# Performance work log

Hardware: AMD Instinct MI355X
Metric: run time of the kernel (lower is better)

Reference implementation:

```python
import jax, jax.numpy as jnp
import numpy as np

B, T, C, HS = 4, 4096, 1024, 64

def setup_inputs() -> dict:
    key = jax.random.key(0)
    kx, kq, kk, kv = jax.random.split(key, 4)
    x = jax.random.normal(kx, (B, T, C), dtype=jnp.float32)
    s = 1.0 / np.sqrt(C)
    Wq = jax.random.normal(kq, (C, HS), dtype=jnp.float32) * s
    Wk = jax.random.normal(kk, (C, HS), dtype=jnp.float32) * s
    Wv = jax.random.normal(kv, (C, HS), dtype=jnp.float32) * s
    return {"x": x, "Wq": Wq, "Wk": Wk, "Wv": Wv}

def reference(x, Wq, Wk, Wv):
    # q,k,v: [B,T,HS]
    q = jnp.einsum('btc,ch->bth', x, Wq)
    k = jnp.einsum('btc,ch,->bth', x, Wk) if False else jnp.einsum('btc,ch->bth', x, Wk)
    v = jnp.einsum('btc,ch->bth', x, Wv)
    dk = q.shape[-1]
    wei = jnp.einsum('bth,bsh->bts', q, k) * (dk ** -0.5)  # [B,T,T]
    Tq = wei.shape[1]
    causal = jnp.tril(jnp.ones((Tq, Tq), dtype=bool))
    wei = jnp.where(causal, wei, -jnp.inf)
    wei = jax.nn.softmax(wei, axis=-1)
    out = jnp.einsum('bts,bsh->bth', wei, v)  # [B,T,HS]
    return out
```

## Files before the change

### kernel.cpp

```cpp
#include <hip/hip_runtime.h>
#include <stdint.h>

typedef __attribute__((ext_vector_type(8))) short short8v;
typedef __attribute__((ext_vector_type(4))) float float4v;

__device__ __forceinline__ unsigned short f32_to_bf16(float f) {
    union { float f; uint32_t u; } v; v.f = f;
    uint32_t u = v.u;
    u += 0x7FFFu + ((u >> 16) & 1u);
    return (unsigned short)(u >> 16);
}

#define T_LEN 4096
#define C_DIM 1024
#define HSZ 64

__global__ void wt_kernel(const float* __restrict__ Wq, const float* __restrict__ Wk,
                          const float* __restrict__ Wv, unsigned short* __restrict__ Wtp) {
    int idx = blockIdx.x * blockDim.x + threadIdx.x;
    int e    = idx & 7;
    int lane = (idx >> 3) & 63;
    int ks   = (idx >> 9) & 31;
    int ct   = idx >> 14;
    int g = lane >> 4, c = lane & 15;
    int k   = ks * 32 + g * 8 + e;
    int col = (ct & 3) * 16 + c;
    int m   = ct >> 2;
    const float* W = (m == 0) ? Wq : ((m == 1) ? Wk : Wv);
    Wtp[idx] = f32_to_bf16(W[(size_t)k * 64 + col]);
}

#define XCH 264

__global__ __launch_bounds__(512) void qkv_kernel(
    const float* __restrict__ x, const unsigned short* __restrict__ Wtp,
    unsigned short* __restrict__ qo, unsigned short* __restrict__ kp,
    unsigned short* __restrict__ vp)
{
    __shared__ __align__(16) unsigned short xs2[2][32 * XCH];
    __shared__ float part[4][2][3][64][4];

    const int tid = threadIdx.x;
    const int bid = (int)blockIdx.x;
    const int batch = (bid >> 1) & 3;
    const int q0    = bid & 1;
    const int hi    = bid >> 3;
    const int rg    = hi * 2 + q0;
    const int row0  = batch * 4096 + rg * 32;

    const int wave = tid >> 6, lane = tid & 63;
    const int wq = wave & 3, wh = wave >> 2;
    const int g = lane >> 4, c = lane & 15;

    float4 ld[4];
    auto LOADX = [&](int cs) {
        #pragma unroll
        for (int i = 0; i < 4; ++i) {
            int f = i * 512 + tid;
            int row = f >> 6, c4 = f & 63;
            ld[i] = *((const float4*)x + (size_t)(row0 + row) * 256 + cs * 64 + c4);
        }
    };
    auto WRITEX = [&](int buf) {
        #pragma unroll
        for (int i = 0; i < 4; ++i) {
            int f = i * 512 + tid;
            int row = f >> 6, c4 = f & 63;
            union { unsigned short s[4]; uint64_t u; } pk;
            pk.s[0] = f32_to_bf16(ld[i].x); pk.s[1] = f32_to_bf16(ld[i].y);
            pk.s[2] = f32_to_bf16(ld[i].z); pk.s[3] = f32_to_bf16(ld[i].w);
            *(uint64_t*)(&xs2[buf][row * XCH + c4 * 4]) = pk.u;
        }
    };

    LOADX(0);
    WRITEX(0);
    __syncthreads();

    float4v acc[2][3];
    #pragma unroll
    for (int rt = 0; rt < 2; ++rt)
        #pragma unroll
        for (int t = 0; t < 3; ++t) acc[rt][t] = (float4v){0,0,0,0};

    const unsigned short* wp0 = Wtp + (size_t)((wq * 3 + 0) * 32) * 512 + lane * 8;
    const unsigned short* wp1 = Wtp + (size_t)((wq * 3 + 1) * 32) * 512 + lane * 8;
    const unsigned short* wp2 = Wtp + (size_t)((wq * 3 + 2) * 32) * 512 + lane * 8;

    for (int cs = 0; cs < 4; ++cs) {
        if (cs < 3) LOADX(cs + 1);
        const int buf = cs & 1;
        #pragma unroll
        for (int ksi = 0; ksi < 4; ++ksi) {
            const int kc = 2 * ksi + wh;
            const int ks = cs * 8 + kc;
            const int koff = kc * 32 + g * 8;
            short8v a0 = *(const short8v*)(&xs2[buf][(0 * 16 + c) * XCH + koff]);
            short8v a1 = *(const short8v*)(&xs2[buf][(1 * 16 + c) * XCH + koff]);
            short8v b0 = *(const short8v*)(wp0 + (size_t)ks * 512);
            short8v b1 = *(const short8v*)(wp1 + (size_t)ks * 512);
            short8v b2 = *(const short8v*)(wp2 + (size_t)ks * 512);
            acc[0][0] = __builtin_amdgcn_mfma_f32_16x16x32_bf16(a0, b0, acc[0][0], 0, 0, 0);
            acc[0][1] = __builtin_amdgcn_mfma_f32_16x16x32_bf16(a0, b1, acc[0][1], 0, 0, 0);
            acc[0][2] = __builtin_amdgcn_mfma_f32_16x16x32_bf16(a0, b2, acc[0][2], 0, 0, 0);
            acc[1][0] = __builtin_amdgcn_mfma_f32_16x16x32_bf16(a1, b0, acc[1][0], 0, 0, 0);
            acc[1][1] = __builtin_amdgcn_mfma_f32_16x16x32_bf16(a1, b1, acc[1][1], 0, 0, 0);
            acc[1][2] = __builtin_amdgcn_mfma_f32_16x16x32_bf16(a1, b2, acc[1][2], 0, 0, 0);
        }
        if (cs < 3) {
            __syncthreads();
            WRITEX(buf ^ 1);
            __syncthreads();
        }
    }

    __syncthreads();
    if (wh == 1) {
        #pragma unroll
        for (int rt = 0; rt < 2; ++rt)
            #pragma unroll
            for (int t = 0; t < 3; ++t)
                #pragma unroll
                for (int j = 0; j < 4; ++j)
                    part[wq][rt][t][lane][j] = acc[rt][t][j];
    }
    __syncthreads();
    if (wh == 0) {
        #pragma unroll
        for (int rt = 0; rt < 2; ++rt) {
            const int row0t = row0 + rt * 16;
            #pragma unroll
            for (int t = 0; t < 3; ++t) {
                float4v av = acc[rt][t];
                #pragma unroll
                for (int j = 0; j < 4; ++j) av[j] += part[wq][rt][t][lane][j];
                int ct = wq * 3 + t;
                int m = ct >> 2, hcol = (ct & 3) * 16 + c;
                if (m == 2) {
                    const int r0 = row0t + g * 4;
                    const int b  = r0 >> 12;
                    const int s0_ = r0 & 4095;
                    const int t2h = s0_ >> 5;
                    const int gv  = (s0_ >> 3) & 3;
                    const int e0  = s0_ & 7;
                    union { unsigned short s[4]; uint64_t u; } pk;
                    #pragma unroll
                    for (int j = 0; j < 4; ++j) pk.s[j] = f32_to_bf16(av[j]);
                    *(uint64_t*)(vp + (size_t)b * 262144 + t2h * 2048 + (ct & 3) * 512
                                    + (gv * 16 + c) * 8 + e0) = pk.u;
                } else if (m == 1) {
                    const int fbase = ((row0t & 4095) >> 6) * 8 + (((row0t & 4095) >> 4) & 3) * 2 + (hcol >> 5);
                    const int b = row0t >> 12;
                    unsigned short* kb = kp + (size_t)b * 262144 + (size_t)fbase * 512
                                         + (((hcol >> 3) & 3) * 16) * 8 + (hcol & 7);
                    #pragma unroll
                    for (int j = 0; j < 4; ++j)
                        kb[(g * 4 + j) * 8] = f32_to_bf16(av[j]);
                } else {
                    float sc = 0.125f;
                    #pragma unroll
                    for (int j = 0; j < 4; ++j)
                        qo[(size_t)(row0t + g * 4 + j) * 64 + hcol] = f32_to_bf16(av[j] * sc);
                }
            }
        }
    }
}

#define PLD 72

__global__ __launch_bounds__(512) void attn_kernel(
    const unsigned short* __restrict__ qi, const unsigned short* __restrict__ kp,
    const unsigned short* __restrict__ vp, float* __restrict__ out)
{
    __shared__ __align__(16) unsigned short Ps[8][16 * PLD];
    __shared__ float CombO[6][16][64];
    __shared__ float CombM[6][16];
    __shared__ float CombL[6][16];

    const int tid   = threadIdx.x;
    const int wave  = tid >> 6, lane = tid & 63;
    const int qh    = wave & 1, slice = wave >> 1;
    const int g = lane >> 4, c = lane & 15;

    const int bid   = (int)blockIdx.x;
    const int batch = (bid >> 1) & 3;
    const int q0    = bid & 1;
    const int m_    = bid >> 3;
    const int mm    = m_ & 31;
    const int qb = q0 ? ((m_ < 32) ? 2 * mm + 1 : 126 - 2 * mm)
                      : ((m_ < 32) ? 2 * mm     : 127 - 2 * mm);

    const int rbase = qb * 32 + qh * 16;
    const size_t bo  = (size_t)batch * T_LEN * HSZ;
    const size_t bov = (size_t)batch * 262144;

    short8v qf0 = *(const short8v*)(qi + bo + (size_t)(rbase + c) * 64 +  0 + g * 8);
    short8v qf1 = *(const short8v*)(qi + bo + (size_t)(rbase + c) * 64 + 32 + g * 8);

    float4v acc[4];
    #pragma unroll
    for (int i2 = 0; i2 < 4; ++i2) acc[i2] = (float4v){0,0,0,0};
    float mrow = -3e38f;
    float lsum = 0.f;

    const int nt_w = ((rbase + 15) >> 6) + 1;
    unsigned short* Pw = &Ps[wave][0];

    short8v kf[8], kn[8];

    auto TILE = [&](int t, const short8v* kb) {
        const int s0 = t * 64;

        float4v sa[4];
        #pragma unroll
        for (int ct = 0; ct < 4; ++ct) {
            float4v z = {0, 0, 0, 0};
            z = __builtin_amdgcn_mfma_f32_16x16x32_bf16(kb[ct * 2 + 0], qf0, z, 0, 0, 0);
            sa[ct] = __builtin_amdgcn_mfma_f32_16x16x32_bf16(kb[ct * 2 + 1], qf1, z, 0, 0, 0);
        }

        short8v vf0[4];
        #pragma unroll
        for (int dt = 0; dt < 4; ++dt)
            vf0[dt] = *(const short8v*)(vp + bov + (size_t)(t * 8 + dt) * 512 + lane * 8);

        if (s0 + 63 > rbase) {
            #pragma unroll
            for (int ct = 0; ct < 4; ++ct)
                #pragma unroll
                for (int j = 0; j < 4; ++j)
                    if (s0 + ct * 16 + g * 4 + j > rbase + c) sa[ct][j] = -3e38f;
        }

        float mx01 = fmaxf(fmaxf(sa[0][0], sa[0][1]), fmaxf(sa[0][2], sa[0][3]));
        float mx11 = fmaxf(fmaxf(sa[1][0], sa[1][1]), fmaxf(sa[1][2], sa[1][3]));
        float mx21 = fmaxf(fmaxf(sa[2][0], sa[2][1]), fmaxf(sa[2][2], sa[2][3]));
        float mx31 = fmaxf(fmaxf(sa[3][0], sa[3][1]), fmaxf(sa[3][2], sa[3][3]));
        float mx = fmaxf(fmaxf(mx01, mx11), fmaxf(mx21, mx31));
        mx = fmaxf(mx, __shfl_xor(mx, 16, 64));
        mx = fmaxf(mx, __shfl_xor(mx, 32, 64));
        const float nm = fmaxf(mrow, mx);
        const float al = __expf(mrow - nm);
        mrow = nm;
        float ps = 0.f;
        #pragma unroll
        for (int ct = 0; ct < 4; ++ct)
            #pragma unroll
            for (int j = 0; j < 4; ++j) {
                float p = __expf(sa[ct][j] - nm);
                sa[ct][j] = p;
                ps += p;
            }
        lsum = lsum * al + ps;
        #pragma unroll
        for (int dt = 0; dt < 4; ++dt)
            #pragma unroll
            for (int j = 0; j < 4; ++j) acc[dt][j] *= al;

        #pragma unroll
        for (int ct = 0; ct < 4; ++ct) {
            union { unsigned short s[4]; uint64_t u; } pk4;
            #pragma unroll
            for (int j = 0; j < 4; ++j) pk4.s[j] = f32_to_bf16(sa[ct][j]);
            *(uint64_t*)(&Pw[c * PLD + ct * 16 + g * 4]) = pk4.u;
        }

        short8v vf1[4];
        #pragma unroll
        for (int dt = 0; dt < 4; ++dt)
            vf1[dt] = *(const short8v*)(vp + bov + (size_t)(t * 8 + 4 + dt) * 512 + lane * 8);

        short8v pa0 = *(const short8v*)(&Pw[c * PLD +  0 + g * 8]);
        short8v pa1 = *(const short8v*)(&Pw[c * PLD + 32 + g * 8]);

        #pragma unroll
        for (int dt = 0; dt < 4; ++dt)
            acc[dt] = __builtin_amdgcn_mfma_f32_16x16x32_bf16(vf0[dt], pa0, acc[dt], 0, 0, 0);
        #pragma unroll
        for (int dt = 0; dt < 4; ++dt)
            acc[dt] = __builtin_amdgcn_mfma_f32_16x16x32_bf16(vf1[dt], pa1, acc[dt], 0, 0, 0);
    };

    auto LOADK = [&](int t, short8v* kd) {
        #pragma unroll
        for (int f = 0; f < 8; ++f)
            kd[f] = *(const short8v*)(kp + bov + (size_t)(t * 8 + f) * 512 + lane * 8);
    };

    int t = slice;
    if (t < nt_w) {
        LOADK(t, kf);
        while (true) {
            const bool h1 = (t + 4 < nt_w);
            if (h1) LOADK(t + 4, kn);
            TILE(t, kf);
            if (!h1) break;
            t += 4;
            const bool h2 = (t + 4 < nt_w);
            if (h2) LOADK(t + 4, kf);
            TILE(t, kn);
            if (!h2) break;
            t += 4;
        }
    }

    lsum += __shfl_xor(lsum, 16, 64);
    lsum += __shfl_xor(lsum, 32, 64);

    if (slice > 0) {
        const int sidx = (slice - 1) * 2 + qh;
        #pragma unroll
        for (int dt = 0; dt < 4; ++dt)
            #pragma unroll
            for (int j = 0; j < 4; ++j)
                CombO[sidx][c][dt * 16 + g * 4 + j] = acc[dt][j];
        if (g == 0) {
            CombM[sidx][c] = mrow;
            CombL[sidx][c] = lsum;
        }
    }
    __syncthreads();

    if (slice == 0) {
        float M = mrow;
        #pragma unroll
        for (int s = 0; s < 3; ++s) M = fmaxf(M, CombM[s * 2 + qh][c]);
        const float a0 = __expf(mrow - M);
        float as[3];
        float lt = lsum * a0;
        #pragma unroll
        for (int s = 0; s < 3; ++s) {
            as[s] = __expf(CombM[s * 2 + qh][c] - M);
            lt += as[s] * CombL[s * 2 + qh][c];
        }
        const float linv = 1.0f / lt;
        #pragma unroll
        for (int dt = 0; dt < 4; ++dt) {
            float4 o;
            float* op = &o.x;
            #pragma unroll
            for (int j = 0; j < 4; ++j) {
                float v = acc[dt][j] * a0;
                #pragma unroll
                for (int s = 0; s < 3; ++s)
                    v += as[s] * CombO[s * 2 + qh][c][dt * 16 + g * 4 + j];
                op[j] = v * linv;
            }
            *(float4*)(out + bo + (size_t)(rbase + c) * 64 + dt * 16 + g * 4) = o;
        }
    }
}

extern "C" void kernel_launch(void* const* d_in, const int* in_sizes, int n_in,
                              void* d_out, int out_size, void* d_ws, size_t ws_size,
                              hipStream_t stream) {
    const float* x  = (const float*)d_in[0];
    const float* Wq = (const float*)d_in[1];
    const float* Wk = (const float*)d_in[2];
    const float* Wv = (const float*)d_in[3];

    unsigned short* Wt = (unsigned short*)d_ws;
    unsigned short* q  = (unsigned short*)((char*)d_ws + (size_t)3 * 65536 * 2);
    unsigned short* kp = q + (size_t)4 * T_LEN * HSZ;
    unsigned short* vp = kp + (size_t)4 * T_LEN * HSZ;
    float* out = (float*)d_out;

    hipLaunchKernelGGL(wt_kernel,  dim3(768), dim3(256), 0, stream, Wq, Wk, Wv, Wt);
    hipLaunchKernelGGL(qkv_kernel, dim3(512), dim3(512), 0, stream, x, Wt, q, kp, vp);
    hipLaunchKernelGGL(attn_kernel, dim3(512), dim3(512), 0, stream, q, kp, vp, out);
}
```

Before: 52.86 us.

## Process both 16-row query halves per wave, sharing K/V tiles across 8 KV slices

```diff
diff --git a/kernel.cpp b/kernel.cpp
--- a/kernel.cpp
+++ b/kernel.cpp
@@ -9,6 +9,10 @@
     uint32_t u = v.u;
     u += 0x7FFFu + ((u >> 16) & 1u);
     return (unsigned short)(u >> 16);
+}
+__device__ __forceinline__ float bf16_to_f32(unsigned short s) {
+    union { uint32_t u; float f; } v; v.u = ((uint32_t)s) << 16;
+    return v.f;
 }
 
 #define T_LEN 4096
@@ -173,76 +177,59 @@
     const unsigned short* __restrict__ qi, const unsigned short* __restrict__ kp,
     const unsigned short* __restrict__ vp, float* __restrict__ out)
 {
-    __shared__ __align__(16) unsigned short Ps[8][16 * PLD];
-    __shared__ float CombO[6][16][64];
-    __shared__ float CombM[6][16];
-    __shared__ float CombL[6][16];
-
-    const int tid   = threadIdx.x;
-    const int wave  = tid >> 6, lane = tid & 63;
-    const int qh    = wave & 1, slice = wave >> 1;
+    __shared__ __align__(16) unsigned short Ps[8][2][16 * PLD];
+    __shared__ unsigned short CombO[2][7][16][64];
+    __shared__ float CombM[2][7][16];
+    __shared__ float CombL[2][7][16];
+
+    const int tid  = threadIdx.x;
+    const int wave = tid >> 6, lane = tid & 63;
     const int g = lane >> 4, c = lane & 15;
 
     const int bid   = (int)blockIdx.x;
+    const int q0    = bid & 1;
     const int batch = (bid >> 1) & 3;
-    const int q0    = bid & 1;
-    const int m_    = bid >> 3;
-    const int mm    = m_ & 31;
-    const int qb = q0 ? ((m_ < 32) ? 2 * mm + 1 : 126 - 2 * mm)
-                      : ((m_ < 32) ? 2 * mm     : 127 - 2 * mm);
-
-    const int rbase = qb * 32 + qh * 16;
+    const int hi    = bid >> 3;
+    const int qb    = 127 - (2 * hi + q0);
+
+    const int rb0 = qb * 32, rb1 = qb * 32 + 16;
+    const int nt0 = ((rb0 + 15) >> 6) + 1;
+    const int nt1 = ((rb1 + 15) >> 6) + 1;
     const size_t bo  = (size_t)batch * T_LEN * HSZ;
     const size_t bov = (size_t)batch * 262144;
 
-    short8v qf0 = *(const short8v*)(qi + bo + (size_t)(rbase + c) * 64 +  0 + g * 8);
-    short8v qf1 = *(const short8v*)(qi + bo + (size_t)(rbase + c) * 64 + 32 + g * 8);
-
-    float4v acc[4];
+    short8v qf00 = *(const short8v*)(qi + bo + (size_t)(rb0 + c) * 64 +  0 + g * 8);
+    short8v qf01 = *(const short8v*)(qi + bo + (size_t)(rb0 + c) * 64 + 32 + g * 8);
+    short8v qf10 = *(const short8v*)(qi + bo + (size_t)(rb1 + c) * 64 +  0 + g * 8);
+    short8v qf11 = *(const short8v*)(qi + bo + (size_t)(rb1 + c) * 64 + 32 + g * 8);
+
+    float4v acc0[4], acc1[4];
     #pragma unroll
-    for (int i2 = 0; i2 < 4; ++i2) acc[i2] = (float4v){0,0,0,0};
-    float mrow = -3e38f;
-    float lsum = 0.f;
-
-    const int nt_w = ((rbase + 15) >> 6) + 1;
-    unsigned short* Pw = &Ps[wave][0];
+    for (int i = 0; i < 4; ++i) { acc0[i] = (float4v){0,0,0,0}; acc1[i] = (float4v){0,0,0,0}; }
+    float m0 = -3e38f, m1 = -3e38f, l0 = 0.f, l1 = 0.f;
+
+    unsigned short* Pw0 = &Ps[wave][0][0];
+    unsigned short* Pw1 = &Ps[wave][1][0];
 
     short8v kf[8], kn[8];
 
-    auto TILE = [&](int t, const short8v* kb) {
-        const int s0 = t * 64;
-
-        float4v sa[4];
-        #pragma unroll
-        for (int ct = 0; ct < 4; ++ct) {
-            float4v z = {0, 0, 0, 0};
-            z = __builtin_amdgcn_mfma_f32_16x16x32_bf16(kb[ct * 2 + 0], qf0, z, 0, 0, 0);
-            sa[ct] = __builtin_amdgcn_mfma_f32_16x16x32_bf16(kb[ct * 2 + 1], qf1, z, 0, 0, 0);
-        }
-
-        short8v vf0[4];
-        #pragma unroll
-        for (int dt = 0; dt < 4; ++dt)
-            vf0[dt] = *(const short8v*)(vp + bov + (size_t)(t * 8 + dt) * 512 + lane * 8);
-
-        if (s0 + 63 > rbase) {
-            #pragma unroll
-            for (int ct = 0; ct < 4; ++ct)
-                #pragma unroll
-                for (int j = 0; j < 4; ++j)
-                    if (s0 + ct * 16 + g * 4 + j > rbase + c) sa[ct][j] = -3e38f;
-        }
-
-        float mx01 = fmaxf(fmaxf(sa[0][0], sa[0][1]), fmaxf(sa[0][2], sa[0][3]));
-        float mx11 = fmaxf(fmaxf(sa[1][0], sa[1][1]), fmaxf(sa[1][2], sa[1][3]));
-        float mx21 = fmaxf(fmaxf(sa[2][0], sa[2][1]), fmaxf(sa[2][2], sa[2][3]));
-        float mx31 = fmaxf(fmaxf(sa[3][0], sa[3][1]), fmaxf(sa[3][2], sa[3][3]));
-        float mx = fmaxf(fmaxf(mx01, mx11), fmaxf(mx21, mx31));
+    auto LOADK = [&](int t, short8v* kd) {
+        #pragma unroll
+        for (int f = 0; f < 8; ++f)
+            kd[f] = *(const short8v*)(kp + bov + (size_t)(t * 8 + f) * 512 + lane * 8);
+    };
+
+    auto SMAX = [&](float4v* sa, float& mr, float& ls, float4v* ac) {
+        float mxA = fmaxf(fmaxf(sa[0][0], sa[0][1]), fmaxf(sa[0][2], sa[0][3]));
+        float mxB = fmaxf(fmaxf(sa[1][0], sa[1][1]), fmaxf(sa[1][2], sa[1][3]));
+        float mxC = fmaxf(fmaxf(sa[2][0], sa[2][1]), fmaxf(sa[2][2], sa[2][3]));
+        float mxD = fmaxf(fmaxf(sa[3][0], sa[3][1]), fmaxf(sa[3][2], sa[3][3]));
+        float mx = fmaxf(fmaxf(mxA, mxB), fmaxf(mxC, mxD));
         mx = fmaxf(mx, __shfl_xor(mx, 16, 64));
         mx = fmaxf(mx, __shfl_xor(mx, 32, 64));
-        const float nm = fmaxf(mrow, mx);
-        const float al = __expf(mrow - nm);
-        mrow = nm;
+        const float nm = fmaxf(mr, mx);
+        const float al = __expf(mr - nm);
+        mr = nm;
         float ps = 0.f;
         #pragma unroll
         for (int ct = 0; ct < 4; ++ct)
@@ -252,12 +239,14 @@
                 sa[ct][j] = p;
                 ps += p;
             }
-        lsum = lsum * al + ps;
-        #pragma unroll
-        for (int dt = 0; dt < 4; ++dt)
-            #pragma unroll
-            for (int j = 0; j < 4; ++j) acc[dt][j] *= al;
-
+        ls = ls * al + ps;
+        #pragma unroll
+        for (int dt = 0; dt < 4; ++dt)
+            #pragma unroll
+            for (int j = 0; j < 4; ++j) ac[dt][j] *= al;
+    };
+
+    auto PWRITE = [&](unsigned short* Pw, const float4v* sa) {
         #pragma unroll
         for (int ct = 0; ct < 4; ++ct) {
             union { unsigned short s[4]; uint64_t u; } pk4;
@@ -265,74 +254,129 @@
             for (int j = 0; j < 4; ++j) pk4.s[j] = f32_to_bf16(sa[ct][j]);
             *(uint64_t*)(&Pw[c * PLD + ct * 16 + g * 4]) = pk4.u;
         }
+    };
+
+    auto TILE2 = [&](int t, const short8v* kb) {
+        const int s0 = t * 64;
+        const bool h0 = t < nt0;
+
+        float4v sa0[4], sa1[4];
+        if (h0) {
+            #pragma unroll
+            for (int ct = 0; ct < 4; ++ct) {
+                float4v z = {0, 0, 0, 0};
+                z = __builtin_amdgcn_mfma_f32_16x16x32_bf16(kb[ct * 2 + 0], qf00, z, 0, 0, 0);
+                sa0[ct] = __builtin_amdgcn_mfma_f32_16x16x32_bf16(kb[ct * 2 + 1], qf01, z, 0, 0, 0);
+            }
+        }
+        #pragma unroll
+        for (int ct = 0; ct < 4; ++ct) {
+            float4v z = {0, 0, 0, 0};
+            z = __builtin_amdgcn_mfma_f32_16x16x32_bf16(kb[ct * 2 + 0], qf10, z, 0, 0, 0);
+            sa1[ct] = __builtin_amdgcn_mfma_f32_16x16x32_bf16(kb[ct * 2 + 1], qf11, z, 0, 0, 0);
+        }
+
+        short8v vf0[4];
+        #pragma unroll
+        for (int dt = 0; dt < 4; ++dt)
+            vf0[dt] = *(const short8v*)(vp + bov + (size_t)(t * 8 + dt) * 512 + lane * 8);
+
+        if (h0 && s0 + 63 > rb0) {
+            #pragma unroll
+            for (int ct = 0; ct < 4; ++ct)
+                #pragma unroll
+                for (int j = 0; j < 4; ++j)
+                    if (s0 + ct * 16 + g * 4 + j > rb0 + c) sa0[ct][j] = -3e38f;
+        }
+        if (s0 + 63 > rb1) {
+            #pragma unroll
+            for (int ct = 0; ct < 4; ++ct)
+                #pragma unroll
+                for (int j = 0; j < 4; ++j)
+                    if (s0 + ct * 16 + g * 4 + j > rb1 + c) sa1[ct][j] = -3e38f;
+        }
+
+        if (h0) SMAX(sa0, m0, l0, acc0);
+        SMAX(sa1, m1, l1, acc1);
+
+        if (h0) PWRITE(Pw0, sa0);
+        PWRITE(Pw1, sa1);
 
         short8v vf1[4];
         #pragma unroll
         for (int dt = 0; dt < 4; ++dt)
             vf1[dt] = *(const short8v*)(vp + bov + (size_t)(t * 8 + 4 + dt) * 512 + lane * 8);
 
-        short8v pa0 = *(const short8v*)(&Pw[c * PLD +  0 + g * 8]);
-        short8v pa1 = *(const short8v*)(&Pw[c * PLD + 32 + g * 8]);
-
-        #pragma unroll
-        for (int dt = 0; dt < 4; ++dt)
-            acc[dt] = __builtin_amdgcn_mfma_f32_16x16x32_bf16(vf0[dt], pa0, acc[dt], 0, 0, 0);
-        #pragma unroll
-        for (int dt = 0; dt < 4; ++dt)
-            acc[dt] = __builtin_amdgcn_mfma_f32_16x16x32_bf16(vf1[dt], pa1, acc[dt], 0, 0, 0);
-    };
-
-    auto LOADK = [&](int t, short8v* kd) {
-        #pragma unroll
-        for (int f = 0; f < 8; ++f)
-            kd[f] = *(const short8v*)(kp + bov + (size_t)(t * 8 + f) * 512 + lane * 8);
-    };
-
-    int t = slice;
-    if (t < nt_w) {
+        short8v pa10 = *(const short8v*)(&Pw1[c * PLD +  0 + g * 8]);
+        short8v pa11 = *(const short8v*)(&Pw1[c * PLD + 32 + g * 8]);
+        #pragma unroll
+        for (int dt = 0; dt < 4; ++dt)
+            acc1[dt] = __builtin_amdgcn_mfma_f32_16x16x32_bf16(vf0[dt], pa10, acc1[dt], 0, 0, 0);
+        #pragma unroll
+        for (int dt = 0; dt < 4; ++dt)
+            acc1[dt] = __builtin_amdgcn_mfma_f32_16x16x32_bf16(vf1[dt], pa11, acc1[dt], 0, 0, 0);
+
+        if (h0) {
+            short8v pa00 = *(const short8v*)(&Pw0[c * PLD +  0 + g * 8]);
+            short8v pa01 = *(const short8v*)(&Pw0[c * PLD + 32 + g * 8]);
+            #pragma unroll
+            for (int dt = 0; dt < 4; ++dt)
+                acc0[dt] = __builtin_amdgcn_mfma_f32_16x16x32_bf16(vf0[dt], pa00, acc0[dt], 0, 0, 0);
+            #pragma unroll
+            for (int dt = 0; dt < 4; ++dt)
+                acc0[dt] = __builtin_amdgcn_mfma_f32_16x16x32_bf16(vf1[dt], pa01, acc0[dt], 0, 0, 0);
+        }
+    };
+
+    int t = wave;
+    if (t < nt1) {
         LOADK(t, kf);
         while (true) {
-            const bool h1 = (t + 4 < nt_w);
-            if (h1) LOADK(t + 4, kn);
-            TILE(t, kf);
+            const bool h1 = (t + 8 < nt1);
+            if (h1) LOADK(t + 8, kn);
+            TILE2(t, kf);
             if (!h1) break;
-            t += 4;
-            const bool h2 = (t + 4 < nt_w);
-            if (h2) LOADK(t + 4, kf);
-            TILE(t, kn);
+            t += 8;
+            const bool h2 = (t + 8 < nt1);
+            if (h2) LOADK(t + 8, kf);
+            TILE2(t, kn);
             if (!h2) break;
-            t += 4;
-        }
-    }
-
-    lsum += __shfl_xor(lsum, 16, 64);
-    lsum += __shfl_xor(lsum, 32, 64);
-
-    if (slice > 0) {
-        const int sidx = (slice - 1) * 2 + qh;
+            t += 8;
+        }
+    }
+
+    l0 += __shfl_xor(l0, 16, 64); l0 += __shfl_xor(l0, 32, 64);
+    l1 += __shfl_xor(l1, 16, 64); l1 += __shfl_xor(l1, 32, 64);
+
+    if (wave != 0) {
         #pragma unroll
         for (int dt = 0; dt < 4; ++dt)
             #pragma unroll
             for (int j = 0; j < 4; ++j)
-                CombO[sidx][c][dt * 16 + g * 4 + j] = acc[dt][j];
-        if (g == 0) {
-            CombM[sidx][c] = mrow;
-            CombL[sidx][c] = lsum;
-        }
+                CombO[0][wave - 1][c][dt * 16 + g * 4 + j] = f32_to_bf16(acc0[dt][j]);
+        if (g == 0) { CombM[0][wave - 1][c] = m0; CombL[0][wave - 1][c] = l0; }
+    }
+    if (wave != 7) {
+        #pragma unroll
+        for (int dt = 0; dt < 4; ++dt)
+            #pragma unroll
+            for (int j = 0; j < 4; ++j)
+                CombO[1][wave][c][dt * 16 + g * 4 + j] = f32_to_bf16(acc1[dt][j]);
+        if (g == 0) { CombM[1][wave][c] = m1; CombL[1][wave][c] = l1; }
     }
     __syncthreads();
 
-    if (slice == 0) {
-        float M = mrow;
-        #pragma unroll
-        for (int s = 0; s < 3; ++s) M = fmaxf(M, CombM[s * 2 + qh][c]);
-        const float a0 = __expf(mrow - M);
-        float as[3];
-        float lt = lsum * a0;
-        #pragma unroll
-        for (int s = 0; s < 3; ++s) {
-            as[s] = __expf(CombM[s * 2 + qh][c] - M);
-            lt += as[s] * CombL[s * 2 + qh][c];
+    auto FINAL = [&](int h, int rb, const float4v* aw, float mw, float lw) {
+        float M = mw;
+        #pragma unroll
+        for (int s = 0; s < 7; ++s) M = fmaxf(M, CombM[h][s][c]);
+        const float a0 = __expf(mw - M);
+        float as[7];
+        float lt = lw * a0;
+        #pragma unroll
+        for (int s = 0; s < 7; ++s) {
+            as[s] = __expf(CombM[h][s][c] - M);
+            lt += as[s] * CombL[h][s][c];
         }
         const float linv = 1.0f / lt;
         #pragma unroll
@@ -341,15 +385,18 @@
             float* op = &o.x;
             #pragma unroll
             for (int j = 0; j < 4; ++j) {
-                float v = acc[dt][j] * a0;
+                float v = aw[dt][j] * a0;
                 #pragma unroll
-                for (int s = 0; s < 3; ++s)
-                    v += as[s] * CombO[s * 2 + qh][c][dt * 16 + g * 4 + j];
+                for (int s = 0; s < 7; ++s)
+                    v += as[s] * bf16_to_f32(CombO[h][s][c][dt * 16 + g * 4 + j]);
                 op[j] = v * linv;
             }
-            *(float4*)(out + bo + (size_t)(rbase + c) * 64 + dt * 16 + g * 4) = o;
-        }
-    }
+            *(float4*)(out + bo + (size_t)(rb + c) * 64 + dt * 16 + g * 4) = o;
+        }
+    };
+
+    if (wave == 0) FINAL(0, rb0, acc0, m0, l0);
+    if (wave == 7) FINAL(1, rb1, acc1, m1, l1);
 }
 
 extern "C" void kernel_launch(void* const* d_in, const int* in_sizes, int n_in,
```

Measured after the change: 56.32 us. +6.6%, slower.

## Enlarge QKV projection tile to 64 rows and alias partial-sum LDS

Applied to the files above, without the earlier changes.

```diff
diff --git a/kernel.cpp b/kernel.cpp
--- a/kernel.cpp
+++ b/kernel.cpp
@@ -9,6 +9,10 @@
     uint32_t u = v.u;
     u += 0x7FFFu + ((u >> 16) & 1u);
     return (unsigned short)(u >> 16);
+}
+__device__ __forceinline__ float bf16_to_f32(unsigned short s) {
+    union { uint32_t u; float f; } v; v.u = ((uint32_t)s) << 16;
+    return v.f;
 }
 
 #define T_LEN 4096
@@ -30,15 +34,16 @@
     Wtp[idx] = f32_to_bf16(W[(size_t)k * 64 + col]);
 }
 
-#define XCH 264
+#define XCH2 136
 
 __global__ __launch_bounds__(512) void qkv_kernel(
     const float* __restrict__ x, const unsigned short* __restrict__ Wtp,
     unsigned short* __restrict__ qo, unsigned short* __restrict__ kp,
     unsigned short* __restrict__ vp)
 {
-    __shared__ __align__(16) unsigned short xs2[2][32 * XCH];
-    __shared__ float part[4][2][3][64][4];
+    __shared__ __align__(16) char smem[4 * 4 * 3 * 64 * 4 * 4];
+    unsigned short (*xs2)[64 * XCH2] = (unsigned short (*)[64 * XCH2])smem;
+    float* part = (float*)smem;
 
     const int tid = threadIdx.x;
     const int bid = (int)blockIdx.x;
@@ -46,7 +51,7 @@
     const int q0    = bid & 1;
     const int hi    = bid >> 3;
     const int rg    = hi * 2 + q0;
-    const int row0  = batch * 4096 + rg * 32;
+    const int row0  = batch * 4096 + rg * 64;
 
     const int wave = tid >> 6, lane = tid & 63;
     const int wq = wave & 3, wh = wave >> 2;
@@ -57,19 +62,19 @@
         #pragma unroll
         for (int i = 0; i < 4; ++i) {
             int f = i * 512 + tid;
-            int row = f >> 6, c4 = f & 63;
-            ld[i] = *((const float4*)x + (size_t)(row0 + row) * 256 + cs * 64 + c4);
+            int row = f >> 5, c4 = f & 31;
+            ld[i] = *((const float4*)x + (size_t)(row0 + row) * 256 + cs * 32 + c4);
         }
     };
     auto WRITEX = [&](int buf) {
         #pragma unroll
         for (int i = 0; i < 4; ++i) {
             int f = i * 512 + tid;
-            int row = f >> 6, c4 = f & 63;
+            int row = f >> 5, c4 = f & 31;
             union { unsigned short s[4]; uint64_t u; } pk;
             pk.s[0] = f32_to_bf16(ld[i].x); pk.s[1] = f32_to_bf16(ld[i].y);
             pk.s[2] = f32_to_bf16(ld[i].z); pk.s[3] = f32_to_bf16(ld[i].w);
-            *(uint64_t*)(&xs2[buf][row * XCH + c4 * 4]) = pk.u;
+            *(uint64_t*)(&xs2[buf][row * XCH2 + c4 * 4]) = pk.u;
         }
     };
 
@@ -77,9 +82,9 @@
     WRITEX(0);
     __syncthreads();
 
-    float4v acc[2][3];
+    float4v acc[4][3];
     #pragma unroll
-    for (int rt = 0; rt < 2; ++rt)
+    for (int rt = 0; rt < 4; ++rt)
         #pragma unroll
         for (int t = 0; t < 3; ++t) acc[rt][t] = (float4v){0,0,0,0};
 
@@ -87,27 +92,26 @@
     const unsigned short* wp1 = Wtp + (size_t)((wq * 3 + 1) * 32) * 512 + lane * 8;
     const unsigned short* wp2 = Wtp + (size_t)((wq * 3 + 2) * 32) * 512 + lane * 8;
 
-    for (int cs = 0; cs < 4; ++cs) {
-        if (cs < 3) LOADX(cs + 1);
+    for (int cs = 0; cs < 8; ++cs) {
+        if (cs < 7) LOADX(cs + 1);
         const int buf = cs & 1;
         #pragma unroll
-        for (int ksi = 0; ksi < 4; ++ksi) {
+        for (int ksi = 0; ksi < 2; ++ksi) {
             const int kc = 2 * ksi + wh;
-            const int ks = cs * 8 + kc;
+            const int ks = cs * 4 + kc;
             const int koff = kc * 32 + g * 8;
-            short8v a0 = *(const short8v*)(&xs2[buf][(0 * 16 + c) * XCH + koff]);
-            short8v a1 = *(const short8v*)(&xs2[buf][(1 * 16 + c) * XCH + koff]);
             short8v b0 = *(const short8v*)(wp0 + (size_t)ks * 512);
             short8v b1 = *(const short8v*)(wp1 + (size_t)ks * 512);
             short8v b2 = *(const short8v*)(wp2 + (size_t)ks * 512);
-            acc[0][0] = __builtin_amdgcn_mfma_f32_16x16x32_bf16(a0, b0, acc[0][0], 0, 0, 0);
-            acc[0][1] = __builtin_amdgcn_mfma_f32_16x16x32_bf16(a0, b1, acc[0][1], 0, 0, 0);
-            acc[0][2] = __builtin_amdgcn_mfma_f32_16x16x32_bf16(a0, b2, acc[0][2], 0, 0, 0);
-            acc[1][0] = __builtin_amdgcn_mfma_f32_16x16x32_bf16(a1, b0, acc[1][0], 0, 0, 0);
-            acc[1][1] = __builtin_amdgcn_mfma_f32_16x16x32_bf16(a1, b1, acc[1][1], 0, 0, 0);
-            acc[1][2] = __builtin_amdgcn_mfma_f32_16x16x32_bf16(a1, b2, acc[1][2], 0, 0, 0);
-        }
-        if (cs < 3) {
+            #pragma unroll
+            for (int rt = 0; rt < 4; ++rt) {
+                short8v a = *(const short8v*)(&xs2[buf][(rt * 16 + c) * XCH2 + koff]);
+                acc[rt][0] = __builtin_amdgcn_mfma_f32_16x16x32_bf16(a, b0, acc[rt][0], 0, 0, 0);
+                acc[rt][1] = __builtin_amdgcn_mfma_f32_16x16x32_bf16(a, b1, acc[rt][1], 0, 0, 0);
+                acc[rt][2] = __builtin_amdgcn_mfma_f32_16x16x32_bf16(a, b2, acc[rt][2], 0, 0, 0);
+            }
+        }
+        if (cs < 7) {
             __syncthreads();
             WRITEX(buf ^ 1);
             __syncthreads();
@@ -117,23 +121,24 @@
     __syncthreads();
     if (wh == 1) {
         #pragma unroll
-        for (int rt = 0; rt < 2; ++rt)
+        for (int rt = 0; rt < 4; ++rt)
             #pragma unroll
             for (int t = 0; t < 3; ++t)
                 #pragma unroll
                 for (int j = 0; j < 4; ++j)
-                    part[wq][rt][t][lane][j] = acc[rt][t][j];
+                    part[(((wq * 4 + rt) * 3 + t) * 64 + lane) * 4 + j] = acc[rt][t][j];
     }
     __syncthreads();
     if (wh == 0) {
         #pragma unroll
-        for (int rt = 0; rt < 2; ++rt) {
+        for (int rt = 0; rt < 4; ++rt) {
             const int row0t = row0 + rt * 16;
             #pragma unroll
             for (int t = 0; t < 3; ++t) {
                 float4v av = acc[rt][t];
                 #pragma unroll
-                for (int j = 0; j < 4; ++j) av[j] += part[wq][rt][t][lane][j];
+                for (int j = 0; j < 4; ++j)
+                    av[j] += part[(((wq * 4 + rt) * 3 + t) * 64 + lane) * 4 + j];
                 int ct = wq * 3 + t;
                 int m = ct >> 2, hcol = (ct & 3) * 16 + c;
                 if (m == 2) {
@@ -367,6 +372,6 @@
     float* out = (float*)d_out;
 
     hipLaunchKernelGGL(wt_kernel,  dim3(768), dim3(256), 0, stream, Wq, Wk, Wv, Wt);
-    hipLaunchKernelGGL(qkv_kernel, dim3(512), dim3(512), 0, stream, x, Wt, q, kp, vp);
+    hipLaunchKernelGGL(qkv_kernel, dim3(256), dim3(512), 0, stream, x, Wt, q, kp, vp);
     hipLaunchKernelGGL(attn_kernel, dim3(512), dim3(512), 0, stream, q, kp, vp, out);
 }
```

New measurement: 56.98 us. 7.8% more time.
